# Kernel tuning notes

Measured on AMD Instinct MI355X. Metric: run time of the kernel, lower is better.

## Reference

```python
import jax, jax.numpy as jnp
import numpy as np

N, IN, H, OUT = 8192, 256, 256, 256
R, MEM, MVD = 2, 128, 128


def setup_inputs() -> dict:
    key = jax.random.key(0)
    ks = jax.random.split(key, 20)
    s = 0.05  # small init scale to keep LSTM activations well-conditioned
    f32 = jnp.float32
    return {
        "inputs": jax.random.normal(ks[0], (N, IN), f32),
        "edges": jax.random.randint(ks[1], (N, 2), 0, N, dtype=jnp.int32),
        "memory": jax.random.normal(ks[2], (N, MVD), f32),
        # input_layer / output_layer
        "Wi": jax.random.normal(ks[3], (H, IN), f32) * s,
        "bi": jnp.zeros((H,), f32),
        "Wo": jax.random.normal(ks[4], (OUT, H), f32) * s,
        "bo": jnp.zeros((OUT,), f32),
        # per-relation edge Linear(2H -> H)
        "edge_W": jax.random.normal(ks[5], (R, H, 2 * H), f32) * s,
        "edge_b": jnp.zeros((R, H), f32),
        # per-relation node LSTM (input = IN + H, hidden = H, 1 layer)
        "node_Wih": jax.random.normal(ks[6], (R, 4 * H, IN + H), f32) * s,
        "node_Whh": jax.random.normal(ks[7], (R, 4 * H, H), f32) * s,
        "node_bih": jnp.zeros((R, 4 * H), f32),
        "node_bhh": jnp.zeros((R, 4 * H), f32),
        # memory Linear(H -> MEM)  [source bug fixed: Linear(2H,...) can't apply to [N,H]]
        "Wm": jax.random.normal(ks[8], (MEM, H), f32) * s,
        "bm": jnp.zeros((MEM,), f32),
        # controller LSTM (input = IN + H + MVD, hidden = H)
        "ctrl_Wih": jax.random.normal(ks[9], (4 * H, IN + H + MVD), f32) * s,
        "ctrl_Whh": jax.random.normal(ks[10], (4 * H, H), f32) * s,
        "ctrl_bih": jnp.zeros((4 * H,), f32),
        "ctrl_bhh": jnp.zeros((4 * H,), f32),
    }


def _lstm(x, Wih, Whh, bih, bhh):
    """PyTorch-style unbatched LSTM over sequence axis 0. x: [T, D] -> [T, H]."""
    Hh = Whh.shape[1]
    xg = x @ Wih.T + bih + bhh  # precompute input contribution [T, 4H]

    def step(carry, xg_t):
        h, c = carry
        g = xg_t + Whh @ h
        i = jax.nn.sigmoid(g[:Hh])
        f = jax.nn.sigmoid(g[Hh:2 * Hh])
        gg = jnp.tanh(g[2 * Hh:3 * Hh])
        o = jax.nn.sigmoid(g[3 * Hh:])
        c = f * c + i * gg
        h = o * jnp.tanh(c)
        return (h, c), h

    init = (jnp.zeros((Hh,), x.dtype), jnp.zeros((Hh,), x.dtype))
    _, hs = jax.lax.scan(step, init, xg)
    return hs


def reference(inputs, edges, memory, Wi, bi, Wo, bo, edge_W, edge_b,
              node_Wih, node_Whh, node_bih, node_bhh, Wm, bm,
              ctrl_Wih, ctrl_Whh, ctrl_bih, ctrl_bhh):
    nodes = inputs @ Wi.T + bi  # [N, H]
    num_rel = edge_W.shape[0]
    for r in range(num_rel):  # small fixed relation count
        # irregular gather of endpoint features, concat, edge Linear
        pair = jnp.concatenate([nodes[edges[:, 0]], nodes[edges[:, 1]]], axis=1)  # [N, 2H]
        edge_h = pair @ edge_W[r].T + edge_b[r]  # [N, H]
        nodes = _lstm(jnp.concatenate([inputs, edge_h], axis=1),
                      node_Wih[r], node_Whh[r], node_bih[r], node_bhh[r])  # [N, H]
    memory_vector = nodes @ Wm.T + bm  # [N, MEM]
    ctrl_in = jnp.concatenate([inputs, nodes, memory], axis=1)  # [N, IN+H+MVD]
    out = _lstm(ctrl_in, ctrl_Wih, ctrl_Whh, ctrl_bih, ctrl_bhh) @ Wo.T + bo  # [N, OUT]
    return (out, memory_vector)
```

## Files before the change

### kernel.cpp

```cpp
#include <hip/hip_runtime.h>


typedef __attribute__((ext_vector_type(8))) short short8;
typedef __attribute__((ext_vector_type(4))) float f32x4;

#define LOG2E 1.44269504088896340736f

__device__ __forceinline__ float fast_sigmoid(float x) {
  float e = __builtin_amdgcn_exp2f(-x * LOG2E);
  return __builtin_amdgcn_rcpf(1.0f + e);
}
__device__ __forceinline__ float fast_tanh(float x) {
  float e = __builtin_amdgcn_exp2f(x * (2.0f * LOG2E));
  return 1.0f - 2.0f * __builtin_amdgcn_rcpf(e + 1.0f);
}

__device__ __forceinline__ unsigned short f2bf(float x) {
  unsigned int u = __float_as_uint(x);
  u += 0x7FFFu + ((u >> 16) & 1u);
  return (unsigned short)(u >> 16);
}

#if __has_builtin(__builtin_amdgcn_sdot4)
#define SDOT4(a, b, c) __builtin_amdgcn_sdot4((a), (b), (c), false)
#else
__device__ __forceinline__ int sdot4_sw(int a, int b, int c) {
  c += ((a << 24) >> 24) * ((b << 24) >> 24);
  c += ((a << 16) >> 24) * ((b << 16) >> 24);
  c += ((a << 8) >> 24) * ((b << 8) >> 24);
  c += (a >> 24) * (b >> 24);
  return c;
}
#define SDOT4(a, b, c) sdot4_sw((a), (b), (c))
#endif

__global__ __launch_bounds__(256) void gemm_bt(
    const unsigned short* __restrict__ A, int lda,
    const unsigned short* __restrict__ W, int ldw,
    const float* __restrict__ bias0,
    const float* __restrict__ bias1,
    void* __restrict__ C, int ldc, int c_f32, int K)
{
  __shared__ unsigned short As[128 * 64];
  __shared__ unsigned short Bs[128 * 64];
  const int tid = threadIdx.x;
  const int lane = tid & 63;
  const int w = tid >> 6;
  const int wm = w >> 1, wn = w & 1;
  const int bm = blockIdx.y * 128, bn = blockIdx.x * 128;

  f32x4 acc[4][4];
#pragma unroll
  for (int m = 0; m < 4; ++m)
#pragma unroll
    for (int n = 0; n < 4; ++n)
      acc[m][n] = (f32x4){0.f, 0.f, 0.f, 0.f};

  for (int k0 = 0; k0 < K; k0 += 64) {
    uint4 va[4], vb[4];
#pragma unroll
    for (int i = 0; i < 4; ++i) {
      int c = i * 256 + tid;
      va[i] = *(const uint4*)(A + (size_t)(bm + (c >> 3)) * lda + k0 + (c & 7) * 8);
      vb[i] = *(const uint4*)(W + (size_t)(bn + (c >> 3)) * ldw + k0 + (c & 7) * 8);
    }
    __syncthreads();
#pragma unroll
    for (int i = 0; i < 4; ++i) {
      int c = i * 256 + tid;
      *(uint4*)&As[c * 8] = va[i];
      *(uint4*)&Bs[c * 8] = vb[i];
    }
    __syncthreads();
#pragma unroll
    for (int ks = 0; ks < 2; ++ks) {
      short8 a[4], b[4];
#pragma unroll
      for (int m = 0; m < 4; ++m)
        a[m] = *(const short8*)&As[(wm * 64 + m * 16 + (lane & 15)) * 64 + ks * 32 + (lane >> 4) * 8];
#pragma unroll
      for (int n = 0; n < 4; ++n)
        b[n] = *(const short8*)&Bs[(wn * 64 + n * 16 + (lane & 15)) * 64 + ks * 32 + (lane >> 4) * 8];
#pragma unroll
      for (int m = 0; m < 4; ++m)
#pragma unroll
        for (int n = 0; n < 4; ++n)
          acc[m][n] = __builtin_amdgcn_mfma_f32_16x16x32_bf16(a[m], b[n], acc[m][n], 0, 0, 0);
    }
  }

#pragma unroll
  for (int n = 0; n < 4; ++n) {
    int col = bn + wn * 64 + n * 16 + (lane & 15);
    float bsum = 0.f;
    if (bias0) bsum += bias0[col];
    if (bias1) bsum += bias1[col];
#pragma unroll
    for (int m = 0; m < 4; ++m) {
      int rbase = bm + wm * 64 + m * 16 + ((lane >> 4) * 4);
#pragma unroll
      for (int q = 0; q < 4; ++q) {
        float v = acc[m][n][q] + bsum;
        if (c_f32)
          ((float*)C)[(size_t)(rbase + q) * ldc + col] = v;
        else
          ((unsigned short*)C)[(size_t)(rbase + q) * ldc + col] = f2bf(v);
      }
    }
  }
}

__global__ void f2bf_flat(const float* __restrict__ src,
                          unsigned short* __restrict__ dst, int n4)
{
  int gid = blockIdx.x * 256 + threadIdx.x;
  if (gid >= n4) return;
  f32x4 v = ((const f32x4*)src)[gid];
  ushort4 o;
  o.x = f2bf(v.x); o.y = f2bf(v.y); o.z = f2bf(v.z); o.w = f2bf(v.w);
  ((ushort4*)dst)[gid] = o;
}

__global__ void f2bf_strided(const float* __restrict__ src,
                             unsigned short* __restrict__ dst, int dstLd,
                             int chunkShift, int total)
{
  int gid = blockIdx.x * 256 + threadIdx.x;
  if (gid >= total) return;
  int row = gid >> chunkShift;
  int ch = gid & ((1 << chunkShift) - 1);
  f32x4 v = ((const f32x4*)src)[(size_t)gid];
  ushort4 o;
  o.x = f2bf(v.x); o.y = f2bf(v.y); o.z = f2bf(v.z); o.w = f2bf(v.w);
  *(ushort4*)(dst + (size_t)row * dstLd + ch * 4) = o;
}

__global__ void quant_rows(const float* __restrict__ Wsrc,
                           int* __restrict__ wqT, float* __restrict__ scales,
                           int nrows)
{
  int row = blockIdx.x * 4 + (threadIdx.x >> 6);
  if (row >= nrows) return;
  int lane = threadIdx.x & 63;
  float v[4];
  float mx = 0.f;
#pragma unroll
  for (int i = 0; i < 4; ++i) {
    v[i] = Wsrc[(size_t)row * 256 + lane * 4 + i];
    mx = fmaxf(mx, fabsf(v[i]));
  }
#pragma unroll
  for (int d = 32; d >= 1; d >>= 1) mx = fmaxf(mx, __shfl_xor(mx, d));
  float inv = (mx > 0.f) ? 127.f / mx : 0.f;
  int packed = 0;
#pragma unroll
  for (int i = 0; i < 4; ++i) {
    int q = __float2int_rn(v[i] * inv);
    q = max(-127, min(127, q));
    packed |= (q & 0xFF) << (8 * i);
  }
  wqT[(size_t)lane * nrows + row] = packed;
  if (lane == 0) scales[row] = mx / 127.f;
}

__global__ __launch_bounds__(512)
__attribute__((amdgpu_waves_per_eu(2, 2)))
void lstm_scan(
    const float* __restrict__ xg,
    const int* __restrict__ wqT,
    const float* __restrict__ wsc,
    unsigned short* __restrict__ hs,
    int T, int ldh)
{
  const int tid = threadIdx.x;
  const int m   = tid >> 1;
  const int odd = tid & 1;
  const int r0  = m + (odd ? 256 : 0);
  const int r1  = m + (odd ? 768 : 512);

  int w0[64], w1[64];
#pragma unroll
  for (int k = 0; k < 64; ++k) w0[k] = wqT[k * 1024 + r0];
#pragma unroll
  for (int k = 0; k < 64; ++k) w1[k] = wqT[k * 1024 + r1];
  const float s0 = wsc[r0] * (1.f / 127.f);
  const float s1 = wsc[r1] * (1.f / 127.f);
  const float A2 = odd ? 1.f : 2.f;
  const float D2 = odd ? 0.f : -1.f;

  __shared__ __align__(16) int hq[2][64];
  if (tid < 64) { hq[0][tid] = 0; hq[1][tid] = 0; }
  float c = 0.f;

  const float* xp = xg;
  float xA0 = xp[r0],        xA1 = xp[r1];
  float xB0 = xp[1024 + r0], xB1 = xp[1024 + r1];
  xp += 2048;

  asm volatile("s_waitcnt lgkmcnt(0)" ::: "memory");
  __builtin_amdgcn_s_barrier();
  asm volatile("" ::: "memory");

#define STEP(T_, RB, X0, X1)                                              \
  {                                                                       \
    float b0 = X0, b1 = X1;                                               \
    X0 = xp[r0]; X1 = xp[r1];    \
    xp += 1024;                                                           \
    int a0 = 0, a1 = 0, a2 = 0, a3 = 0;                                   \
    const int4* hb = (const int4*)hq[RB];                                 \
    _Pragma("unroll")                                                     \
    for (int kk = 0; kk < 16; ++kk) {                                     \
      int4 hc = hb[kk];                         \
      a0 = SDOT4(w0[4 * kk + 0], hc.x, a0);                               \
      a1 = SDOT4(w0[4 * kk + 1], hc.y, a1);                               \
      a0 = SDOT4(w0[4 * kk + 2], hc.z, a0);                               \
      a1 = SDOT4(w0[4 * kk + 3], hc.w, a1);                               \
      a2 = SDOT4(w1[4 * kk + 0], hc.x, a2);                               \
      a3 = SDOT4(w1[4 * kk + 1], hc.y, a3);                               \
      a2 = SDOT4(w1[4 * kk + 2], hc.z, a2);                               \
      a3 = SDOT4(w1[4 * kk + 3], hc.w, a3);                               \
    }                                                                     \
    float pa = (float)(a0 + a1) * s0 + b0;                                \
    float pb = (float)(a2 + a3) * s1 + b1;                                \
    float first  = fast_sigmoid(pa);              \
    float second = A2 * fast_sigmoid(A2 * pb) + D2;           \
    float u  = first * second;                            \
    float un = __shfl_xor(u, 1);                   \
    c = first * c + un;                              \
    float h = second * fast_tanh(c);                  \
    if (odd) {                                                            \
      hs[(size_t)(T_) * ldh + m] = f2bf(h);                               \
      int q = __float2int_rn(h * 127.f);                                  \
      q = max(-127, min(127, q));                                         \
      ((char*)hq[RB ^ 1])[m] = (char)q;                                   \
    }                                                                     \
    asm volatile("s_waitcnt lgkmcnt(0)" ::: "memory");                    \
    __builtin_amdgcn_s_barrier();                                         \
    asm volatile("" ::: "memory");                                        \
  }

  for (int t = 0; t < T; t += 2) {
    STEP(t, 0, xA0, xA1);
    STEP(t + 1, 1, xB0, xB1);
  }
#undef STEP
}

__global__ void gather_pair(const unsigned short* __restrict__ nodes,
                            const int* __restrict__ edges,
                            unsigned short* __restrict__ pair)
{
  int gid = blockIdx.x * 256 + threadIdx.x;
  int row = gid >> 6;
  int ch = gid & 63;
  int side = ch >> 5;
  int k = ch & 31;
  int src = edges[row * 2 + side];
  uint4 v = ((const uint4*)(nodes + (size_t)src * 256))[k];
  ((uint4*)(pair + (size_t)row * 512))[ch] = v;
}

extern "C" void kernel_launch(void* const* d_in, const int* in_sizes, int n_in,
                              void* d_out, int out_size, void* d_ws, size_t ws_size,
                              hipStream_t stream)
{
  const float* inputs   = (const float*)d_in[0];
  const int*   edges    = (const int*)d_in[1];
  const float* memory   = (const float*)d_in[2];
  const float* Wi       = (const float*)d_in[3];
  const float* bi       = (const float*)d_in[4];
  const float* Wo       = (const float*)d_in[5];
  const float* bo       = (const float*)d_in[6];
  const float* edge_W   = (const float*)d_in[7];
  const float* edge_b   = (const float*)d_in[8];
  const float* node_Wih = (const float*)d_in[9];
  const float* node_Whh = (const float*)d_in[10];
  const float* node_bih = (const float*)d_in[11];
  const float* node_bhh = (const float*)d_in[12];
  const float* Wm       = (const float*)d_in[13];
  const float* bm       = (const float*)d_in[14];
  const float* cWih     = (const float*)d_in[15];
  const float* cWhh     = (const float*)d_in[16];
  const float* cbih     = (const float*)d_in[17];
  const float* cbhh     = (const float*)d_in[18];

  char* ws = (char*)d_ws;
  float*          xgbuf  = (float*)(ws + 0);
  unsigned short* Xbf    = (unsigned short*)(ws + 33554432);
  unsigned short* Xc     = (unsigned short*)(ws + 41943040);
  unsigned short* nodes0 = (unsigned short*)(ws + 52428800);
  unsigned short* nodesA = (unsigned short*)(ws + 56623104);
  unsigned short* PAIR   = (unsigned short*)(ws + 60817408);
  unsigned short* hsC    = (unsigned short*)(ws + 69206016);
  unsigned short* WiB    = (unsigned short*)(ws + 73400320);
  unsigned short* WoB    = (unsigned short*)(ws + 73531392);
  unsigned short* eWB    = (unsigned short*)(ws + 73662464);
  unsigned short* nWihB  = (unsigned short*)(ws + 74186752);
  unsigned short* WmB    = (unsigned short*)(ws + 76283904);
  unsigned short* cWihB  = (unsigned short*)(ws + 76349440);
  int*            wqN0   = (int*)(ws + 77660160);
  int*            wqN1   = (int*)(ws + 77922304);
  int*            wqC    = (int*)(ws + 78184448);
  float*          scN0   = (float*)(ws + 78446592);
  float*          scN1   = (float*)(ws + 78450688);
  float*          scC    = (float*)(ws + 78454784);

  float* out0 = (float*)d_out;
  float* out1 = out0 + 8192 * 256;

  quant_rows<<<256, 256, 0, stream>>>(node_Whh, wqN0, scN0, 1024);
  quant_rows<<<256, 256, 0, stream>>>(node_Whh + 1024 * 256, wqN1, scN1, 1024);
  quant_rows<<<256, 256, 0, stream>>>(cWhh, wqC, scC, 1024);
  f2bf_flat<<<64, 256, 0, stream>>>(Wi, WiB, 16384);
  f2bf_flat<<<64, 256, 0, stream>>>(Wo, WoB, 16384);
  f2bf_flat<<<256, 256, 0, stream>>>(edge_W, eWB, 65536);
  f2bf_flat<<<1024, 256, 0, stream>>>(node_Wih, nWihB, 262144);
  f2bf_flat<<<32, 256, 0, stream>>>(Wm, WmB, 8192);
  f2bf_flat<<<640, 256, 0, stream>>>(cWih, cWihB, 163840);

  f2bf_strided<<<2048, 256, 0, stream>>>(inputs, Xbf, 512, 6, 8192 * 64);
  f2bf_strided<<<2048, 256, 0, stream>>>(inputs, Xc, 640, 6, 8192 * 64);
  f2bf_strided<<<1024, 256, 0, stream>>>(memory, Xc + 512, 640, 5, 8192 * 32);

  gemm_bt<<<dim3(2, 64), 256, 0, stream>>>(Xbf, 512, WiB, 256, bi, nullptr,
                                           nodes0, 256, 0, 256);

  gather_pair<<<2048, 256, 0, stream>>>(nodes0, edges, PAIR);
  gemm_bt<<<dim3(2, 64), 256, 0, stream>>>(PAIR, 512, eWB, 512, edge_b, nullptr,
                                           Xbf + 256, 512, 0, 512);
  gemm_bt<<<dim3(8, 64), 256, 0, stream>>>(Xbf, 512, nWihB, 512, node_bih, node_bhh,
                                           xgbuf, 1024, 1, 512);
  lstm_scan<<<1, 512, 0, stream>>>(xgbuf, wqN0, scN0, nodesA, 8192, 256);

  gather_pair<<<2048, 256, 0, stream>>>(nodesA, edges, PAIR);
  gemm_bt<<<dim3(2, 64), 256, 0, stream>>>(PAIR, 512, eWB + 256 * 512, 512,
                                           edge_b + 256, nullptr, Xbf + 256, 512, 0, 512);
  gemm_bt<<<dim3(8, 64), 256, 0, stream>>>(Xbf, 512, nWihB + 1024 * 512, 512,
                                           node_bih + 1024, node_bhh + 1024,
                                           xgbuf, 1024, 1, 512);
  lstm_scan<<<1, 512, 0, stream>>>(xgbuf, wqN1, scN1, Xc + 256, 8192, 640);

  gemm_bt<<<dim3(1, 64), 256, 0, stream>>>(Xc + 256, 640, WmB, 256, bm, nullptr,
                                           out1, 128, 1, 256);

  gemm_bt<<<dim3(8, 64), 256, 0, stream>>>(Xc, 640, cWihB, 640, cbih, cbhh,
                                           xgbuf, 1024, 1, 640);
  lstm_scan<<<1, 512, 0, stream>>>(xgbuf, wqC, scC, hsC, 8192, 256);

  gemm_bt<<<dim3(2, 64), 256, 0, stream>>>(hsC, 256, WoB, 256, bo, nullptr,
                                           out0, 256, 1, 256);
}
```

Before: 19.89 ms.

## Split LSTM scan dot products across four lanes with shuffle reduction

The recurrent LSTM scan now runs 1024 threads instead of 512. Each group of four lanes splits the K dimension of the recurrent matvec across all four gates, holding 64 packed weights per thread instead of 128. Partial sums are combined with cross-lane shuffles, and one lane per hidden unit updates the cell state. The aim is to shorten the serial dot-product chain per step, at the cost of more shuffles and a barrier across twice as many waves every timestep.

```diff
diff --git a/kernel.cpp b/kernel.cpp
--- a/kernel.cpp
+++ b/kernel.cpp
@@ -163,8 +163,7 @@
   if (lane == 0) scales[row] = mx / 127.f;
 }
 
-__global__ __launch_bounds__(512)
-__attribute__((amdgpu_waves_per_eu(2, 2)))
+__global__ __launch_bounds__(1024)
 void lstm_scan(
     const float* __restrict__ xg,
     const int* __restrict__ wqT,
@@ -172,67 +171,84 @@
     unsigned short* __restrict__ hs,
     int T, int ldh)
 {
-  const int tid = threadIdx.x;
-  const int m   = tid >> 1;
-  const int odd = tid & 1;
-  const int r0  = m + (odd ? 256 : 0);
-  const int r1  = m + (odd ? 768 : 512);
-
-  int w0[64], w1[64];
-#pragma unroll
-  for (int k = 0; k < 64; ++k) w0[k] = wqT[k * 1024 + r0];
-#pragma unroll
-  for (int k = 0; k < 64; ++k) w1[k] = wqT[k * 1024 + r1];
-  const float s0 = wsc[r0] * (1.f / 127.f);
-  const float s1 = wsc[r1] * (1.f / 127.f);
-  const float A2 = odd ? 1.f : 2.f;
-  const float D2 = odd ? 0.f : -1.f;
+  const int tid  = threadIdx.x;
+  const int unit = tid >> 2;
+  const int s    = tid & 3;
+  const int row  = s * 256 + unit;
+
+  int w[4][16];
+#pragma unroll
+  for (int j = 0; j < 4; ++j)
+#pragma unroll
+    for (int kk = 0; kk < 16; ++kk)
+      w[j][kk] = wqT[(s * 16 + kk) * 1024 + ((s ^ j) << 8) + unit];
+#pragma unroll
+  for (int j = 0; j < 4; ++j)
+#pragma unroll
+    for (int kk = 0; kk < 16; ++kk)
+      asm("" : "+v"(w[j][kk]));
+
+  const float sc = wsc[row] * (1.f / 127.f);
+  const float A2 = (s == 2) ? 2.f : 1.f;
+  const float D2 = (s == 2) ? -1.f : 0.f;
 
   __shared__ __align__(16) int hq[2][64];
   if (tid < 64) { hq[0][tid] = 0; hq[1][tid] = 0; }
   float c = 0.f;
 
   const float* xp = xg;
-  float xA0 = xp[r0],        xA1 = xp[r1];
-  float xB0 = xp[1024 + r0], xB1 = xp[1024 + r1];
+  float xA = xp[row];
+  float xB = xp[1024 + row];
   xp += 2048;
 
-  asm volatile("s_waitcnt lgkmcnt(0)" ::: "memory");
-  __builtin_amdgcn_s_barrier();
-  asm volatile("" ::: "memory");
-
-#define STEP(T_, RB, X0, X1)                                              \
+  __syncthreads();
+
+#define STEP(T_, HB, HBN, X)                                              \
   {                                                                       \
-    float b0 = X0, b1 = X1;                                               \
-    X0 = xp[r0]; X1 = xp[r1];    \
+    float xcur = X;                                                       \
+    X = xp[row];                    \
     xp += 1024;                                                           \
     int a0 = 0, a1 = 0, a2 = 0, a3 = 0;                                   \
-    const int4* hb = (const int4*)hq[RB];                                 \
     _Pragma("unroll")                                                     \
-    for (int kk = 0; kk < 16; ++kk) {                                     \
-      int4 hc = hb[kk];                         \
-      a0 = SDOT4(w0[4 * kk + 0], hc.x, a0);                               \
-      a1 = SDOT4(w0[4 * kk + 1], hc.y, a1);                               \
-      a0 = SDOT4(w0[4 * kk + 2], hc.z, a0);                               \
-      a1 = SDOT4(w0[4 * kk + 3], hc.w, a1);                               \
-      a2 = SDOT4(w1[4 * kk + 0], hc.x, a2);                               \
-      a3 = SDOT4(w1[4 * kk + 1], hc.y, a3);                               \
-      a2 = SDOT4(w1[4 * kk + 2], hc.z, a2);                               \
-      a3 = SDOT4(w1[4 * kk + 3], hc.w, a3);                               \
+    for (int kt = 0; kt < 4; ++kt) {                                      \
+      int4 hc = ((const int4*)(HB))[s * 4 + kt];                          \
+      a0 = SDOT4(w[0][kt * 4 + 0], hc.x, a0);                             \
+      a1 = SDOT4(w[1][kt * 4 + 0], hc.x, a1);                             \
+      a2 = SDOT4(w[2][kt * 4 + 0], hc.x, a2);                             \
+      a3 = SDOT4(w[3][kt * 4 + 0], hc.x, a3);                             \
+      a0 = SDOT4(w[0][kt * 4 + 1], hc.y, a0);                             \
+      a1 = SDOT4(w[1][kt * 4 + 1], hc.y, a1);                             \
+      a2 = SDOT4(w[2][kt * 4 + 1], hc.y, a2);                             \
+      a3 = SDOT4(w[3][kt * 4 + 1], hc.y, a3);                             \
+      a0 = SDOT4(w[0][kt * 4 + 2], hc.z, a0);                             \
+      a1 = SDOT4(w[1][kt * 4 + 2], hc.z, a1);                             \
+      a2 = SDOT4(w[2][kt * 4 + 2], hc.z, a2);                             \
+      a3 = SDOT4(w[3][kt * 4 + 2], hc.z, a3);                             \
+      a0 = SDOT4(w[0][kt * 4 + 3], hc.w, a0);                             \
+      a1 = SDOT4(w[1][kt * 4 + 3], hc.w, a1);                             \
+      a2 = SDOT4(w[2][kt * 4 + 3], hc.w, a2);                             \
+      a3 = SDOT4(w[3][kt * 4 + 3], hc.w, a3);                             \
     }                                                                     \
-    float pa = (float)(a0 + a1) * s0 + b0;                                \
-    float pb = (float)(a2 + a3) * s1 + b1;                                \
-    float first  = fast_sigmoid(pa);              \
-    float second = A2 * fast_sigmoid(A2 * pb) + D2;           \
-    float u  = first * second;                            \
-    float un = __shfl_xor(u, 1);                   \
-    c = first * c + un;                              \
-    float h = second * fast_tanh(c);                  \
-    if (odd) {                                                            \
-      hs[(size_t)(T_) * ldh + m] = f2bf(h);                               \
+          \
+    {                                                                     \
+      int v0 = __shfl_xor(a1, 1), v1 = __shfl_xor(a0, 1);                 \
+      int v2 = __shfl_xor(a3, 1), v3 = __shfl_xor(a2, 1);                 \
+      a0 += v0; a1 += v1; a2 += v2; a3 += v3;                             \
+      v0 = __shfl_xor(a2, 2); v1 = __shfl_xor(a3, 2);                     \
+      a0 += v0; a1 += v1;                                                 \
+    }                                                                     \
+    float p = fmaf((float)a0, sc, xcur);             \
+    float act = A2 * fast_sigmoid(A2 * p) + D2;                           \
+    float cross = __shfl_xor(act, 2);               \
+    float u = act * cross;                               \
+    float un = __shfl_xor(u, 1);                       \
+    if (s == 1) {                                     \
+      c = fmaf(act, c, un);                                               \
+      float h = cross * fast_tanh(c);                                     \
+      hs[(size_t)(T_) * ldh + unit] = f2bf(h);                            \
       int q = __float2int_rn(h * 127.f);                                  \
       q = max(-127, min(127, q));                                         \
-      ((char*)hq[RB ^ 1])[m] = (char)q;                                   \
+      ((char*)(HBN))[unit] = (char)q;                                     \
     }                                                                     \
     asm volatile("s_waitcnt lgkmcnt(0)" ::: "memory");                    \
     __builtin_amdgcn_s_barrier();                                         \
@@ -240,8 +256,8 @@
   }
 
   for (int t = 0; t < T; t += 2) {
-    STEP(t, 0, xA0, xA1);
-    STEP(t + 1, 1, xB0, xB1);
+    STEP(t,     hq[0], hq[1], xA);
+    STEP(t + 1, hq[1], hq[0], xB);
   }
 #undef STEP
 }
@@ -330,7 +346,7 @@
                                            Xbf + 256, 512, 0, 512);
   gemm_bt<<<dim3(8, 64), 256, 0, stream>>>(Xbf, 512, nWihB, 512, node_bih, node_bhh,
                                            xgbuf, 1024, 1, 512);
-  lstm_scan<<<1, 512, 0, stream>>>(xgbuf, wqN0, scN0, nodesA, 8192, 256);
+  lstm_scan<<<1, 1024, 0, stream>>>(xgbuf, wqN0, scN0, nodesA, 8192, 256);
 
   gather_pair<<<2048, 256, 0, stream>>>(nodesA, edges, PAIR);
   gemm_bt<<<dim3(2, 64), 256, 0, stream>>>(PAIR, 512, eWB + 256 * 512, 512,
@@ -338,14 +354,14 @@
   gemm_bt<<<dim3(8, 64), 256, 0, stream>>>(Xbf, 512, nWihB + 1024 * 512, 512,
                                            node_bih + 1024, node_bhh + 1024,
                                            xgbuf, 1024, 1, 512);
-  lstm_scan<<<1, 512, 0, stream>>>(xgbuf, wqN1, scN1, Xc + 256, 8192, 640);
+  lstm_scan<<<1, 1024, 0, stream>>>(xgbuf, wqN1, scN1, Xc + 256, 8192, 640);
 
   gemm_bt<<<dim3(1, 64), 256, 0, stream>>>(Xc + 256, 640, WmB, 256, bm, nullptr,
                                            out1, 128, 1, 256);
 
   gemm_bt<<<dim3(8, 64), 256, 0, stream>>>(Xc, 640, cWihB, 640, cbih, cbhh,
                                            xgbuf, 1024, 1, 640);
-  lstm_scan<<<1, 512, 0, stream>>>(xgbuf, wqC, scC, hsC, 8192, 256);
+  lstm_scan<<<1, 1024, 0, stream>>>(xgbuf, wqC, scC, hsC, 8192, 256);
 
   gemm_bt<<<dim3(2, 64), 256, 0, stream>>>(hsC, 256, WoB, 256, bo, nullptr,
                                            out0, 256, 1, 256);
```

Result: slower. 22.03 ms (+10.8%).

## Use int8 MFMA for LSTM recurrent matvec with gate-interleaved weight layout

Applied to the files above, without the earlier changes.

Replaces the per-thread sdot4 recurrent matvec in the serial LSTM scan with v_mfma_i32_16x16x64_i8 matrix instructions on pre-packed int8 weight fragments. The gate rows are permuted so each unit's four gates (i, f, g, o) land in one lane, which removes the cross-lane shuffle. Input weights, biases and scales are permuted to match. The goal is to shorten the per-timestep critical path of the scan. In exchange, the MFMA computes a full 16-column product where only one column is useful, picks results through masked selects, and adds several small preprocessing kernels.

```diff
diff --git a/kernel.cpp b/kernel.cpp
--- a/kernel.cpp
+++ b/kernel.cpp
@@ -3,6 +3,7 @@
 
 typedef __attribute__((ext_vector_type(8))) short short8;
 typedef __attribute__((ext_vector_type(4))) float f32x4;
+typedef __attribute__((ext_vector_type(4))) int i32x4;
 
 #define LOG2E 1.44269504088896340736f
 
@@ -21,17 +22,18 @@
   return (unsigned short)(u >> 16);
 }
 
-#if __has_builtin(__builtin_amdgcn_sdot4)
-#define SDOT4(a, b, c) __builtin_amdgcn_sdot4((a), (b), (c), false)
+#if __has_builtin(__builtin_amdgcn_mfma_i32_16x16x64_i8)
+#define MFMA_I8(a, b, c) __builtin_amdgcn_mfma_i32_16x16x64_i8((a), (b), (c), 0, 0, 0)
+#define MFMA_FENCE()
 #else
-__device__ __forceinline__ int sdot4_sw(int a, int b, int c) {
-  c += ((a << 24) >> 24) * ((b << 24) >> 24);
-  c += ((a << 16) >> 24) * ((b << 16) >> 24);
-  c += ((a << 8) >> 24) * ((b << 8) >> 24);
-  c += (a >> 24) * (b >> 24);
-  return c;
-}
-#define SDOT4(a, b, c) sdot4_sw((a), (b), (c))
+__device__ __forceinline__ i32x4 mfma_i8_asm(i32x4 a, i32x4 b, i32x4 c) {
+  i32x4 d;
+  asm volatile("v_mfma_i32_16x16x64_i8 %0, %1, %2, %3"
+               : "=v"(d) : "v"(a), "v"(b), "v"(c));
+  return d;
+}
+#define MFMA_I8(a, b, c) mfma_i8_asm((a), (b), (c))
+#define MFMA_FENCE() asm volatile("s_nop 7\ns_nop 7" ::: "memory")
 #endif
 
 __global__ __launch_bounds__(256) void gemm_bt(
@@ -135,113 +137,166 @@
   *(ushort4*)(dst + (size_t)row * dstLd + ch * 4) = o;
 }
 
-__global__ void quant_rows(const float* __restrict__ Wsrc,
-                           int* __restrict__ wqT, float* __restrict__ scales,
-                           int nrows)
+__global__ void f2bf_perm(const float* __restrict__ src,
+                          unsigned short* __restrict__ dst, int K)
+{
+  int rowp = blockIdx.x;
+  int orig = (rowp & 3) * 256 + (rowp >> 2);
+  int t = threadIdx.x;
+  if (t * 4 >= K) return;
+  f32x4 v = *(const f32x4*)(src + (size_t)orig * K + t * 4);
+  ushort4 o;
+  o.x = f2bf(v.x); o.y = f2bf(v.y); o.z = f2bf(v.z); o.w = f2bf(v.w);
+  *(ushort4*)(dst + (size_t)rowp * K + t * 4) = o;
+}
+
+__global__ void row_scale(const float* __restrict__ Wsrc,
+                          float* __restrict__ scR, int nrows)
 {
   int row = blockIdx.x * 4 + (threadIdx.x >> 6);
   if (row >= nrows) return;
   int lane = threadIdx.x & 63;
-  float v[4];
   float mx = 0.f;
 #pragma unroll
+  for (int i = 0; i < 4; ++i)
+    mx = fmaxf(mx, fabsf(Wsrc[(size_t)row * 256 + lane * 4 + i]));
+#pragma unroll
+  for (int d = 32; d >= 1; d >>= 1) mx = fmaxf(mx, __shfl_xor(mx, d));
+  if (lane == 0) scR[row] = mx / 127.f;
+}
+
+__global__ void scale_fold(const float* __restrict__ scR,
+                           float* __restrict__ scF)
+{
+  int i = blockIdx.x * 256 + threadIdx.x;
+  if (i >= 1024) return;
+  int orig = (i & 3) * 256 + (i >> 2);
+  scF[i] = scR[orig] * (1.f / 127.f);
+}
+
+__global__ void bias_perm(const float* __restrict__ b1,
+                          const float* __restrict__ b2,
+                          float* __restrict__ pb)
+{
+  int i = blockIdx.x * 256 + threadIdx.x;
+  if (i >= 1024) return;
+  int orig = (i & 3) * 256 + (i >> 2);
+  pb[i] = b1[orig] + b2[orig];
+}
+
+__global__ void pack_mfma(const float* __restrict__ Wsrc,
+                          const float* __restrict__ scR,
+                          int* __restrict__ apk)
+{
+  int gid = blockIdx.x * 256 + threadIdx.x;
+  int tid = gid >> 7, idx = gid & 127;
+  int w = tid >> 6, l = tid & 63;
+  int rr = idx >> 4, c = (idx >> 2) & 3, e = idx & 3;
+  int rowp = (w * 8 + rr) * 16 + (l & 15);
+  int orig = (rowp & 3) * 256 + (rowp >> 2);
+  int kb = c * 64 + ((l >> 4) << 4) + e * 4;
+  float s = scR[orig];
+  float inv = (s > 0.f) ? 1.f / s : 0.f;
+  const float* src = Wsrc + (size_t)orig * 256 + kb;
+  int packed = 0;
+#pragma unroll
   for (int i = 0; i < 4; ++i) {
-    v[i] = Wsrc[(size_t)row * 256 + lane * 4 + i];
-    mx = fmaxf(mx, fabsf(v[i]));
-  }
-#pragma unroll
-  for (int d = 32; d >= 1; d >>= 1) mx = fmaxf(mx, __shfl_xor(mx, d));
-  float inv = (mx > 0.f) ? 127.f / mx : 0.f;
-  int packed = 0;
-#pragma unroll
-  for (int i = 0; i < 4; ++i) {
-    int q = __float2int_rn(v[i] * inv);
+    int q = __float2int_rn(src[i] * inv);
     q = max(-127, min(127, q));
     packed |= (q & 0xFF) << (8 * i);
   }
-  wqT[(size_t)lane * nrows + row] = packed;
-  if (lane == 0) scales[row] = mx / 127.f;
+  apk[gid] = packed;
 }
 
 __global__ __launch_bounds__(512)
-__attribute__((amdgpu_waves_per_eu(2, 2)))
 void lstm_scan(
     const float* __restrict__ xg,
-    const int* __restrict__ wqT,
-    const float* __restrict__ wsc,
+    const i32x4* __restrict__ apk,
+    const float* __restrict__ scF,
     unsigned short* __restrict__ hs,
     int T, int ldh)
 {
   const int tid = threadIdx.x;
-  const int m   = tid >> 1;
-  const int odd = tid & 1;
-  const int r0  = m + (odd ? 256 : 0);
-  const int r1  = m + (odd ? 768 : 512);
-
-  int w0[64], w1[64];
-#pragma unroll
-  for (int k = 0; k < 64; ++k) w0[k] = wqT[k * 1024 + r0];
-#pragma unroll
-  for (int k = 0; k < 64; ++k) w1[k] = wqT[k * 1024 + r1];
-  const float s0 = wsc[r0] * (1.f / 127.f);
-  const float s1 = wsc[r1] * (1.f / 127.f);
-  const float A2 = odd ? 1.f : 2.f;
-  const float D2 = odd ? 0.f : -1.f;
-
-  __shared__ __align__(16) int hq[2][64];
-  if (tid < 64) { hq[0][tid] = 0; hq[1][tid] = 0; }
-  float c = 0.f;
-
-  const float* xp = xg;
-  float xA0 = xp[r0],        xA1 = xp[r1];
-  float xB0 = xp[1024 + r0], xB1 = xp[1024 + r1];
-  xp += 2048;
-
-  asm volatile("s_waitcnt lgkmcnt(0)" ::: "memory");
-  __builtin_amdgcn_s_barrier();
-  asm volatile("" ::: "memory");
-
-#define STEP(T_, RB, X0, X1)                                              \
+  const int w = tid >> 6;
+  const int l = tid & 63;
+  const int g = l >> 4;
+  const int cc = l & 15;
+  const int rt = cc >> 1;
+  const int u = (w * 8 + rt) * 4 + g;
+  const bool active = (cc & 1) == 0;
+
+  i32x4 a[8][4];
+  {
+    const i32x4* ap = apk + (size_t)tid * 32;
+#pragma unroll
+    for (int rr = 0; rr < 8; ++rr)
+#pragma unroll
+      for (int c = 0; c < 4; ++c)
+        a[rr][c] = ap[rr * 4 + c];
+  }
+  const f32x4 sc = *(const f32x4*)(scF + u * 4);
+  bool msk[8];
+#pragma unroll
+  for (int i = 0; i < 8; ++i) msk[i] = (rt == i);
+
+  __shared__ __align__(16) char hqb[2][256];
+  if (tid < 128) ((int*)hqb)[tid] = 0;
+  float cst = 0.f;
+  const i32x4 zero = (i32x4){0, 0, 0, 0};
+
+  f32x4 xcur = *(const f32x4*)(xg + u * 4);
+  __syncthreads();
+
+#define STEP(T_, RB, WB)                                                  \
   {                                                                       \
-    float b0 = X0, b1 = X1;                                               \
-    X0 = xp[r0]; X1 = xp[r1];    \
-    xp += 1024;                                                           \
-    int a0 = 0, a1 = 0, a2 = 0, a3 = 0;                                   \
-    const int4* hb = (const int4*)hq[RB];                                 \
+    f32x4 xnext = *(const f32x4*)(xg + (size_t)((T_) + 1) * 1024 + u * 4);\
+    i32x4 b0 = *(const i32x4*)(&hqb[RB][0 * 64 + g * 16]);                \
+    i32x4 b1 = *(const i32x4*)(&hqb[RB][1 * 64 + g * 16]);                \
+    i32x4 b2 = *(const i32x4*)(&hqb[RB][2 * 64 + g * 16]);                \
+    i32x4 b3 = *(const i32x4*)(&hqb[RB][3 * 64 + g * 16]);                \
+    i32x4 acc[8];                                                         \
     _Pragma("unroll")                                                     \
-    for (int kk = 0; kk < 16; ++kk) {                                     \
-      int4 hc = hb[kk];                         \
-      a0 = SDOT4(w0[4 * kk + 0], hc.x, a0);                               \
-      a1 = SDOT4(w0[4 * kk + 1], hc.y, a1);                               \
-      a0 = SDOT4(w0[4 * kk + 2], hc.z, a0);                               \
-      a1 = SDOT4(w0[4 * kk + 3], hc.w, a1);                               \
-      a2 = SDOT4(w1[4 * kk + 0], hc.x, a2);                               \
-      a3 = SDOT4(w1[4 * kk + 1], hc.y, a3);                               \
-      a2 = SDOT4(w1[4 * kk + 2], hc.z, a2);                               \
-      a3 = SDOT4(w1[4 * kk + 3], hc.w, a3);                               \
+    for (int rr = 0; rr < 8; ++rr) {                                      \
+      i32x4 d = MFMA_I8(a[rr][0], b0, zero);                              \
+      d = MFMA_I8(a[rr][1], b1, d);                                       \
+      d = MFMA_I8(a[rr][2], b2, d);                                       \
+      d = MFMA_I8(a[rr][3], b3, d);                                       \
+      acc[rr] = d;                                                        \
     }                                                                     \
-    float pa = (float)(a0 + a1) * s0 + b0;                                \
-    float pb = (float)(a2 + a3) * s1 + b1;                                \
-    float first  = fast_sigmoid(pa);              \
-    float second = A2 * fast_sigmoid(A2 * pb) + D2;           \
-    float u  = first * second;                            \
-    float un = __shfl_xor(u, 1);                   \
-    c = first * c + un;                              \
-    float h = second * fast_tanh(c);                  \
-    if (odd) {                                                            \
-      hs[(size_t)(T_) * ldh + m] = f2bf(h);                               \
+    MFMA_FENCE();                                                         \
+    i32x4 sel = acc[0];                                                   \
+    _Pragma("unroll")                                                     \
+    for (int i = 1; i < 8; ++i) {                                         \
+      sel.x = msk[i] ? acc[i].x : sel.x;                                  \
+      sel.y = msk[i] ? acc[i].y : sel.y;                                  \
+      sel.z = msk[i] ? acc[i].z : sel.z;                                  \
+      sel.w = msk[i] ? acc[i].w : sel.w;                                  \
+    }                                                                     \
+    float pi = fmaf((float)sel.x, sc.x, xcur.x);                          \
+    float pf = fmaf((float)sel.y, sc.y, xcur.y);                          \
+    float pg = fmaf((float)sel.z, sc.z, xcur.z);                          \
+    float po = fmaf((float)sel.w, sc.w, xcur.w);                          \
+    float ii = fast_sigmoid(pi);                                          \
+    float ff = fast_sigmoid(pf);                                          \
+    float gg = fast_tanh(pg);                                             \
+    float oo = fast_sigmoid(po);                                          \
+    cst = fmaf(ff, cst, ii * gg);                                         \
+    float h = oo * fast_tanh(cst);                                        \
+    if (active) {                                                         \
+      hs[(size_t)(T_) * ldh + u] = f2bf(h);                               \
       int q = __float2int_rn(h * 127.f);                                  \
       q = max(-127, min(127, q));                                         \
-      ((char*)hq[RB ^ 1])[m] = (char)q;                                   \
+      hqb[WB][u] = (char)q;                                               \
     }                                                                     \
+    xcur = xnext;                                                         \
     asm volatile("s_waitcnt lgkmcnt(0)" ::: "memory");                    \
     __builtin_amdgcn_s_barrier();                                         \
     asm volatile("" ::: "memory");                                        \
   }
 
   for (int t = 0; t < T; t += 2) {
-    STEP(t, 0, xA0, xA1);
-    STEP(t + 1, 1, xB0, xB1);
+    STEP(t, 0, 1);
+    STEP(t + 1, 1, 0);
   }
 #undef STEP
 }
@@ -298,25 +353,41 @@
   unsigned short* nWihB  = (unsigned short*)(ws + 74186752);
   unsigned short* WmB    = (unsigned short*)(ws + 76283904);
   unsigned short* cWihB  = (unsigned short*)(ws + 76349440);
-  int*            wqN0   = (int*)(ws + 77660160);
-  int*            wqN1   = (int*)(ws + 77922304);
-  int*            wqC    = (int*)(ws + 78184448);
-  float*          scN0   = (float*)(ws + 78446592);
-  float*          scN1   = (float*)(ws + 78450688);
-  float*          scC    = (float*)(ws + 78454784);
+  int*            apkN0  = (int*)(ws + 77660160);
+  int*            apkN1  = (int*)(ws + 77922304);
+  int*            apkC   = (int*)(ws + 78184448);
+  float*          scF0   = (float*)(ws + 78446592);
+  float*          scF1   = (float*)(ws + 78450688);
+  float*          scFC   = (float*)(ws + 78454784);
+  float*          scR0   = (float*)(ws + 78458880);
+  float*          scR1   = (float*)(ws + 78462976);
+  float*          scR2   = (float*)(ws + 78467072);
+  float*          pb0    = (float*)(ws + 78471168);
+  float*          pb1    = (float*)(ws + 78475264);
+  float*          pbC    = (float*)(ws + 78479360);
 
   float* out0 = (float*)d_out;
   float* out1 = out0 + 8192 * 256;
 
-  quant_rows<<<256, 256, 0, stream>>>(node_Whh, wqN0, scN0, 1024);
-  quant_rows<<<256, 256, 0, stream>>>(node_Whh + 1024 * 256, wqN1, scN1, 1024);
-  quant_rows<<<256, 256, 0, stream>>>(cWhh, wqC, scC, 1024);
+  row_scale<<<256, 256, 0, stream>>>(node_Whh, scR0, 1024);
+  row_scale<<<256, 256, 0, stream>>>(node_Whh + 1024 * 256, scR1, 1024);
+  row_scale<<<256, 256, 0, stream>>>(cWhh, scR2, 1024);
+  pack_mfma<<<256, 256, 0, stream>>>(node_Whh, scR0, apkN0);
+  pack_mfma<<<256, 256, 0, stream>>>(node_Whh + 1024 * 256, scR1, apkN1);
+  pack_mfma<<<256, 256, 0, stream>>>(cWhh, scR2, apkC);
+  scale_fold<<<4, 256, 0, stream>>>(scR0, scF0);
+  scale_fold<<<4, 256, 0, stream>>>(scR1, scF1);
+  scale_fold<<<4, 256, 0, stream>>>(scR2, scFC);
+  bias_perm<<<4, 256, 0, stream>>>(node_bih, node_bhh, pb0);
+  bias_perm<<<4, 256, 0, stream>>>(node_bih + 1024, node_bhh + 1024, pb1);
+  bias_perm<<<4, 256, 0, stream>>>(cbih, cbhh, pbC);
   f2bf_flat<<<64, 256, 0, stream>>>(Wi, WiB, 16384);
   f2bf_flat<<<64, 256, 0, stream>>>(Wo, WoB, 16384);
   f2bf_flat<<<256, 256, 0, stream>>>(edge_W, eWB, 65536);
-  f2bf_flat<<<1024, 256, 0, stream>>>(node_Wih, nWihB, 262144);
   f2bf_flat<<<32, 256, 0, stream>>>(Wm, WmB, 8192);
-  f2bf_flat<<<640, 256, 0, stream>>>(cWih, cWihB, 163840);
+  f2bf_perm<<<1024, 256, 0, stream>>>(node_Wih, nWihB, 512);
+  f2bf_perm<<<1024, 256, 0, stream>>>(node_Wih + 1024 * 512, nWihB + 1024 * 512, 512);
+  f2bf_perm<<<1024, 256, 0, stream>>>(cWih, cWihB, 640);
 
   f2bf_strided<<<2048, 256, 0, stream>>>(inputs, Xbf, 512, 6, 8192 * 64);
   f2bf_strided<<<2048, 256, 0, stream>>>(inputs, Xc, 640, 6, 8192 * 64);
@@ -328,24 +399,23 @@
   gather_pair<<<2048, 256, 0, stream>>>(nodes0, edges, PAIR);
   gemm_bt<<<dim3(2, 64), 256, 0, stream>>>(PAIR, 512, eWB, 512, edge_b, nullptr,
                                            Xbf + 256, 512, 0, 512);
-  gemm_bt<<<dim3(8, 64), 256, 0, stream>>>(Xbf, 512, nWihB, 512, node_bih, node_bhh,
+  gemm_bt<<<dim3(8, 64), 256, 0, stream>>>(Xbf, 512, nWihB, 512, pb0, nullptr,
                                            xgbuf, 1024, 1, 512);
-  lstm_scan<<<1, 512, 0, stream>>>(xgbuf, wqN0, scN0, nodesA, 8192, 256);
+  lstm_scan<<<1, 512, 0, stream>>>(xgbuf, (const i32x4*)apkN0, scF0, nodesA, 8192, 256);
 
   gather_pair<<<2048, 256, 0, stream>>>(nodesA, edges, PAIR);
   gemm_bt<<<dim3(2, 64), 256, 0, stream>>>(PAIR, 512, eWB + 256 * 512, 512,
                                            edge_b + 256, nullptr, Xbf + 256, 512, 0, 512);
   gemm_bt<<<dim3(8, 64), 256, 0, stream>>>(Xbf, 512, nWihB + 1024 * 512, 512,
-                                           node_bih + 1024, node_bhh + 1024,
-                                           xgbuf, 1024, 1, 512);
-  lstm_scan<<<1, 512, 0, stream>>>(xgbuf, wqN1, scN1, Xc + 256, 8192, 640);
+                                           pb1, nullptr, xgbuf, 1024, 1, 512);
+  lstm_scan<<<1, 512, 0, stream>>>(xgbuf, (const i32x4*)apkN1, scF1, Xc + 256, 8192, 640);
 
   gemm_bt<<<dim3(1, 64), 256, 0, stream>>>(Xc + 256, 640, WmB, 256, bm, nullptr,
                                            out1, 128, 1, 256);
 
-  gemm_bt<<<dim3(8, 64), 256, 0, stream>>>(Xc, 640, cWihB, 640, cbih, cbhh,
+  gemm_bt<<<dim3(8, 64), 256, 0, stream>>>(Xc, 640, cWihB, 640, pbC, nullptr,
                                            xgbuf, 1024, 1, 640);
-  lstm_scan<<<1, 512, 0, stream>>>(xgbuf, wqC, scC, hsC, 8192, 256);
+  lstm_scan<<<1, 512, 0, stream>>>(xgbuf, (const i32x4*)apkC, scFC, hsC, 8192, 256);
 
   gemm_bt<<<dim3(2, 64), 256, 0, stream>>>(hsC, 256, WoB, 256, bo, nullptr,
                                            out0, 256, 1, 256);
```

Result: faster. 17.70 ms (-11.0%).
